# Kernel optimization log

Measured on AMD Instinct MI355X. Metric: run time of the kernel, lower is better.

## Reference

```python
import jax, jax.numpy as jnp
import numpy as np

B, T, J = 256, 150, 25  # batch, time_step, num_joints (NTU-style skeleton)
K_LIST = (2, 3, 4)      # k values from the source loop -> 3 stats each -> topo_feat_dim = 9


def setup_inputs() -> dict:
    key = jax.random.key(0)
    x = jax.random.normal(key, (B, T, J, 3), dtype=jnp.float32)
    return {"x": x}


def _pairwise_dist(pos):
    # pos: [B,T,J,3] -> dist: [B,T,J,J], safe sqrt so grad at zero diagonal is 0
    diff = pos[:, :, :, None, :] - pos[:, :, None, :, :]          # [B,T,J,J,3]
    s = jnp.sum(diff * diff, axis=-1)                              # [B,T,J,J]
    return jnp.where(s > 0, jnp.sqrt(jnp.where(s > 0, s, 1.0)), 0.0)


def reference(x) -> jnp.ndarray:
    # Faithful, fully vectorized version of the topo-feature block of
    # FiveStreamMaha_GCN_Model.forward (per-frame cdist + kNN + stats),
    # batched over all frames instead of Python loops over t and k.
    pos = x[..., :3]                     # [B,T,J,3]
    dist = _pairwise_dist(pos)           # [B,T,J,J]

    feats = []
    for k in K_LIST:
        actual_k = min(k, J - 1)
        # smallest (actual_k+1) distances; drop self (distance 0 at index 0)
        neg_vals, _ = jax.lax.top_k(-dist, actual_k + 1)   # [B,T,J,k+1], descending in -d
        knn_d = -neg_vals[..., 1:actual_k + 1]             # [B,T,J,k], ascending distances
        avg_dist = jnp.mean(knn_d, axis=-1)                # [B,T,J]
        std_dist = jnp.std(knn_d, axis=-1, ddof=1)         # torch.std default: unbiased
        min_dist = jnp.min(knn_d, axis=-1)                 # [B,T,J]
        k_feat = jnp.stack([avg_dist, std_dist, min_dist], axis=-1)  # [B,T,J,3]
        feats.append(jnp.mean(k_feat, axis=1))             # mean over time -> [B,J,3]

    return jnp.concatenate(feats, axis=-1)                 # [B,J,9]
```

## Files before the change

kernel.cpp:

```cpp
#include <hip/hip_runtime.h>
#include <cfloat>

#define NB 256
#define NT 150
#define NJ 25
#define HALF_T 75
#define SLOTS 16
#define ITERS 5
#define BLOCKSZ 256

#define FSQRT(x) __builtin_amdgcn_sqrtf(x)

#define INS4(s0, s1, s2, s3, v)                                   \
    {                                                             \
        float m_;                                                 \
        m_ = fminf(s0, v); v = fmaxf(s0, v); s0 = m_;             \
        m_ = fminf(s1, v); v = fmaxf(s1, v); s1 = m_;             \
        m_ = fminf(s2, v); v = fmaxf(s2, v); s2 = m_;             \
        s3 = fminf(s3, v);                                        \
    }

__device__ __forceinline__ void features(float r0, float r1, float r2, float r3,
                                         float* f) {
    const float d1 = FSQRT(r0), d2 = FSQRT(r1), d3 = FSQRT(r2), d4 = FSQRT(r3);
    const float rs2 = r0 + r1, rs3 = rs2 + r2, rs4 = rs3 + r3;
    const float s2 = d1 + d2, a2f = 0.5f * s2;
    const float s3 = s2 + d3, a3f = s3 * (1.0f / 3.0f);
    const float s4 = s3 + d4, a4f = 0.25f * s4;
    f[0] = a2f;
    f[1] = FSQRT(fmaxf(rs2 - 2.0f * a2f * a2f, 0.0f));
    f[2] = a3f;
    f[3] = FSQRT(fmaxf((rs3 - 3.0f * a3f * a3f) * 0.5f, 0.0f));
    f[4] = a4f;
    f[5] = FSQRT(fmaxf((rs4 - 4.0f * a4f * a4f) * (1.0f / 3.0f), 0.0f));
    f[6] = d1;
}

__global__ __launch_bounds__(BLOCKSZ, 4) void knn_feat(
        const float* __restrict__ x, float* __restrict__ ws) {
    __shared__ float4 spos[SLOTS][NJ];
    __shared__ float  red[4][16][14];

    const int tid  = threadIdx.x;
    const int wave = tid >> 6;
    const int lane = tid & 63;
    const int q    = (lane >> 4) & 3;
    const int k    = lane & 15;
    const int slot = wave * 4 + q;
    const int jj0  = min(2 * k, NJ - 1);
    const int jj1  = min(2 * k + 1, NJ - 1);

    const int blk = blockIdx.x;
    const int b   = blk >> 1;
    const int h   = blk & 1;
    const float* xb = x + (size_t)(b * NT + h * HALF_T) * NJ * 3;

    float acc0[7], acc1[7];
#pragma unroll
    for (int f = 0; f < 7; ++f) { acc0[f] = 0.0f; acc1[f] = 0.0f; }

#pragma unroll 1
    for (int it = 0; it < ITERS; ++it) {
#pragma unroll
        for (int turn = 0; turn < 2; ++turn) {
            const int t = tid + turn * BLOCKSZ;
            if (t < SLOTS * NJ) {
                const int fl = t / NJ;
                const int j  = t - fl * NJ;
                const int gf = min(it * SLOTS + fl, HALF_T - 1);
                const float* s = xb + (size_t)(gf * NJ + j) * 3;
                spos[fl][j] = make_float4(s[0], s[1], s[2], 0.0f);
            }
        }
        __syncthreads();

        const float4 own0 = spos[slot][jj0];
        const float4 own1 = spos[slot][jj1];

        float a0 = FLT_MAX, a1 = FLT_MAX, a2 = FLT_MAX, a3 = FLT_MAX;
        float e0 = FLT_MAX, e1 = FLT_MAX, e2 = FLT_MAX, e3 = FLT_MAX;
#pragma unroll
        for (int i = 0; i < NJ; ++i) {
            const float4 c = spos[slot][i];
            float dx = c.x - own0.x, dy = c.y - own0.y, dz = c.z - own0.z;
            float d20 = dx * dx + dy * dy + dz * dz;
            dx = c.x - own1.x; dy = c.y - own1.y; dz = c.z - own1.z;
            float d21 = dx * dx + dy * dy + dz * dz;
            d20 = (i == jj0) ? FLT_MAX : d20;
            d21 = (i == jj1) ? FLT_MAX : d21;
            INS4(a0, a1, a2, a3, d20);
            INS4(e0, e1, e2, e3, d21);
        }

        float f0[7], f1[7];
        features(a0, a1, a2, a3, f0);
        features(e0, e1, e2, e3, f1);

        const float vm = (it * SLOTS + slot < HALF_T) ? 1.0f : 0.0f;
#pragma unroll
        for (int f = 0; f < 7; ++f) {
            acc0[f] = fmaf(vm, f0[f], acc0[f]);
            acc1[f] = fmaf(vm, f1[f], acc1[f]);
        }
        __syncthreads();
    }

#pragma unroll
    for (int f = 0; f < 7; ++f) {
        acc0[f] += __shfl_xor(acc0[f], 16, 64);
        acc0[f] += __shfl_xor(acc0[f], 32, 64);
        acc1[f] += __shfl_xor(acc1[f], 16, 64);
        acc1[f] += __shfl_xor(acc1[f], 32, 64);
    }
    if (lane < 16) {
#pragma unroll
        for (int f = 0; f < 7; ++f) {
            red[wave][k][f]     = acc0[f];
            red[wave][k][7 + f] = acc1[f];
        }
    }
    __syncthreads();

    if (tid < 16 * 14) {
        const int k2   = tid / 14;
        const int rest = tid - k2 * 14;
        const int which = rest / 7;
        const int f    = rest - which * 7;
        const int j    = 2 * k2 + which;
        if (j < NJ) {
            const float s = red[0][k2][rest] + red[1][k2][rest] +
                            red[2][k2][rest] + red[3][k2][rest];
            ws[(size_t)((b * 2 + h) * NJ + j) * 7 + f] = s * (1.0f / (float)NT);
        }
    }
}

__global__ __launch_bounds__(BLOCKSZ) void final_kernel(
        const float* __restrict__ ws, float* __restrict__ out) {
    const int o = blockIdx.x * blockDim.x + threadIdx.x;
    if (o >= NB * NJ * 9) return;
    const int f9 = o % 9;
    const int bj = o / 9;
    const int j  = bj % NJ;
    const int b  = bj / NJ;
    const int f7 = (f9 % 3 == 2) ? 6 : (f9 / 3) * 2 + (f9 % 3);
    const size_t i0 = (size_t)((b * 2 + 0) * NJ + j) * 7 + f7;
    const size_t i1 = (size_t)((b * 2 + 1) * NJ + j) * 7 + f7;
    out[o] = ws[i0] + ws[i1];
}

extern "C" void kernel_launch(void* const* d_in, const int* in_sizes, int n_in,
                              void* d_out, int out_size, void* d_ws, size_t ws_size,
                              hipStream_t stream) {
    const float* x = (const float*)d_in[0];
    float* out = (float*)d_out;
    float* ws = (float*)d_ws;

    knn_feat<<<NB * 2, BLOCKSZ, 0, stream>>>(x, ws);
    final_kernel<<<(NB * NJ * 9 + BLOCKSZ - 1) / BLOCKSZ, BLOCKSZ, 0, stream>>>(ws, out);
}
```

Before: 74.27 us.

## Split time axis into 10 tiles per batch to raise block-level parallelism

Instead of 2 blocks per batch each looping 5 times over 16-frame chunks, each block now handles one 15-frame tile, giving 2560 blocks with no serial loop. The final kernel sums the 10 per-tile partials instead of 2. This targets the small grid and serialized load/sync/compute chain, at the cost of more blocks, more workspace traffic, and wasting 1 of 16 slots per tile. The launch bound is raised to 8 blocks per CU.

```diff
diff --git a/kernel.cpp b/kernel.cpp
--- a/kernel.cpp
+++ b/kernel.cpp
@@ -4,9 +4,9 @@
 #define NB 256
 #define NT 150
 #define NJ 25
-#define HALF_T 75
+#define FPB 15
+#define TILES (NT / FPB)
 #define SLOTS 16
-#define ITERS 5
 #define BLOCKSZ 256
 
 #define FSQRT(x) __builtin_amdgcn_sqrtf(x)
@@ -36,7 +36,7 @@
     f[6] = d1;
 }
 
-__global__ __launch_bounds__(BLOCKSZ, 4) void knn_feat(
+__global__ __launch_bounds__(BLOCKSZ, 8) void knn_feat(
         const float* __restrict__ x, float* __restrict__ ws) {
     __shared__ float4 spos[SLOTS][NJ];
     __shared__ float  red[4][16][14];
@@ -50,59 +50,52 @@
     const int jj0  = min(2 * k, NJ - 1);
     const int jj1  = min(2 * k + 1, NJ - 1);
 
-    const int blk = blockIdx.x;
-    const int b   = blk >> 1;
-    const int h   = blk & 1;
-    const float* xb = x + (size_t)(b * NT + h * HALF_T) * NJ * 3;
+    const int blk   = blockIdx.x;
+    const int batch = blk / TILES;
+    const int tile  = blk - batch * TILES;
+    const int t0    = tile * FPB;
 
+#pragma unroll
+    for (int turn = 0; turn < 2; ++turn) {
+        const int t = tid + turn * BLOCKSZ;
+        if (t < SLOTS * NJ) {
+            const int fl = t / NJ;
+            const int j  = t - fl * NJ;
+            const int gf = min(t0 + fl, NT - 1);
+            const float* s = x + (size_t)((batch * NT + gf) * NJ + j) * 3;
+            spos[fl][j] = make_float4(s[0], s[1], s[2], 0.0f);
+        }
+    }
+    __syncthreads();
+
+    const float4 own0 = spos[slot][jj0];
+    const float4 own1 = spos[slot][jj1];
+
+    float a0 = FLT_MAX, a1 = FLT_MAX, a2 = FLT_MAX, a3 = FLT_MAX;
+    float e0 = FLT_MAX, e1 = FLT_MAX, e2 = FLT_MAX, e3 = FLT_MAX;
+#pragma unroll
+    for (int i = 0; i < NJ; ++i) {
+        const float4 c = spos[slot][i];
+        float dx = c.x - own0.x, dy = c.y - own0.y, dz = c.z - own0.z;
+        float d20 = dx * dx + dy * dy + dz * dz;
+        dx = c.x - own1.x; dy = c.y - own1.y; dz = c.z - own1.z;
+        float d21 = dx * dx + dy * dy + dz * dz;
+        d20 = (i == jj0) ? FLT_MAX : d20;
+        d21 = (i == jj1) ? FLT_MAX : d21;
+        INS4(a0, a1, a2, a3, d20);
+        INS4(e0, e1, e2, e3, d21);
+    }
+
+    float f0[7], f1[7];
+    features(a0, a1, a2, a3, f0);
+    features(e0, e1, e2, e3, f1);
+
+    const float vm = (slot < FPB) ? 1.0f : 0.0f;
     float acc0[7], acc1[7];
 #pragma unroll
-    for (int f = 0; f < 7; ++f) { acc0[f] = 0.0f; acc1[f] = 0.0f; }
-
-#pragma unroll 1
-    for (int it = 0; it < ITERS; ++it) {
-#pragma unroll
-        for (int turn = 0; turn < 2; ++turn) {
-            const int t = tid + turn * BLOCKSZ;
-            if (t < SLOTS * NJ) {
-                const int fl = t / NJ;
-                const int j  = t - fl * NJ;
-                const int gf = min(it * SLOTS + fl, HALF_T - 1);
-                const float* s = xb + (size_t)(gf * NJ + j) * 3;
-                spos[fl][j] = make_float4(s[0], s[1], s[2], 0.0f);
-            }
-        }
-        __syncthreads();
-
-        const float4 own0 = spos[slot][jj0];
-        const float4 own1 = spos[slot][jj1];
-
-        float a0 = FLT_MAX, a1 = FLT_MAX, a2 = FLT_MAX, a3 = FLT_MAX;
-        float e0 = FLT_MAX, e1 = FLT_MAX, e2 = FLT_MAX, e3 = FLT_MAX;
-#pragma unroll
-        for (int i = 0; i < NJ; ++i) {
-            const float4 c = spos[slot][i];
-            float dx = c.x - own0.x, dy = c.y - own0.y, dz = c.z - own0.z;
-            float d20 = dx * dx + dy * dy + dz * dz;
-            dx = c.x - own1.x; dy = c.y - own1.y; dz = c.z - own1.z;
-            float d21 = dx * dx + dy * dy + dz * dz;
-            d20 = (i == jj0) ? FLT_MAX : d20;
-            d21 = (i == jj1) ? FLT_MAX : d21;
-            INS4(a0, a1, a2, a3, d20);
-            INS4(e0, e1, e2, e3, d21);
-        }
-
-        float f0[7], f1[7];
-        features(a0, a1, a2, a3, f0);
-        features(e0, e1, e2, e3, f1);
-
-        const float vm = (it * SLOTS + slot < HALF_T) ? 1.0f : 0.0f;
-#pragma unroll
-        for (int f = 0; f < 7; ++f) {
-            acc0[f] = fmaf(vm, f0[f], acc0[f]);
-            acc1[f] = fmaf(vm, f1[f], acc1[f]);
-        }
-        __syncthreads();
+    for (int f = 0; f < 7; ++f) {
+        acc0[f] = vm * f0[f];
+        acc1[f] = vm * f1[f];
     }
 
 #pragma unroll
@@ -122,15 +115,15 @@
     __syncthreads();
 
     if (tid < 16 * 14) {
-        const int k2   = tid / 14;
-        const int rest = tid - k2 * 14;
+        const int k2    = tid / 14;
+        const int rest  = tid - k2 * 14;
         const int which = rest / 7;
-        const int f    = rest - which * 7;
-        const int j    = 2 * k2 + which;
+        const int f     = rest - which * 7;
+        const int j     = 2 * k2 + which;
         if (j < NJ) {
             const float s = red[0][k2][rest] + red[1][k2][rest] +
                             red[2][k2][rest] + red[3][k2][rest];
-            ws[(size_t)((b * 2 + h) * NJ + j) * 7 + f] = s * (1.0f / (float)NT);
+            ws[(size_t)blk * 175 + j * 7 + f] = s * (1.0f / (float)NT);
         }
     }
 }
@@ -144,9 +137,11 @@
     const int j  = bj % NJ;
     const int b  = bj / NJ;
     const int f7 = (f9 % 3 == 2) ? 6 : (f9 / 3) * 2 + (f9 % 3);
-    const size_t i0 = (size_t)((b * 2 + 0) * NJ + j) * 7 + f7;
-    const size_t i1 = (size_t)((b * 2 + 1) * NJ + j) * 7 + f7;
-    out[o] = ws[i0] + ws[i1];
+    const float* p = ws + (size_t)b * TILES * 175 + j * 7 + f7;
+    float s = 0.0f;
+#pragma unroll
+    for (int t = 0; t < TILES; ++t) s += p[t * 175];
+    out[o] = s;
 }
 
 extern "C" void kernel_launch(void* const* d_in, const int* in_sizes, int n_in,
@@ -156,6 +151,6 @@
     float* out = (float*)d_out;
     float* ws = (float*)d_ws;
 
-    knn_feat<<<NB * 2, BLOCKSZ, 0, stream>>>(x, ws);
+    knn_feat<<<NB * TILES, BLOCKSZ, 0, stream>>>(x, ws);
     final_kernel<<<(NB * NJ * 9 + BLOCKSZ - 1) / BLOCKSZ, BLOCKSZ, 0, stream>>>(ws, out);
 }
```

Measured after the change: 71.68 us (median of 2 runs). 1.04x faster.
